# Kernel optimization log

Measured on AMD Instinct MI355X. Metric: run time of the kernel, lower is better.

The kernel has to match this reference:

```python
import jax, jax.numpy as jnp
import numpy as np

MIN_NORM = 1e-15
EPS = 1e-7
N_NODES = 100000
N_EDGES = 1600000
D_IN = 256
D_OUT = 128

# ---- Hyperboloid manifold ops (HGCN-style) ----

def proj_tan0(u, c):
    # zero out the time (first) coordinate
    return jnp.concatenate([jnp.zeros_like(u[..., :1]), u[..., 1:]], axis=-1)

def proj(x, c):
    # project onto hyperboloid: recompute time coord from space coords
    K = 1.0 / c
    y = x[..., 1:]
    t = jnp.sqrt(jnp.clip(K + jnp.sum(y * y, axis=-1, keepdims=True), EPS, None))
    return jnp.concatenate([t, y], axis=-1)

def expmap0(u, c):
    sqrtK = jnp.sqrt(1.0 / c)
    x = u[..., 1:]
    nrm = jnp.clip(jnp.linalg.norm(x, axis=-1, keepdims=True), MIN_NORM, None)
    theta = nrm / sqrtK
    t0 = sqrtK * jnp.cosh(theta)
    rest = sqrtK * jnp.sinh(theta) * x / nrm
    return proj(jnp.concatenate([t0, rest], axis=-1), c)

def logmap0(x, c):
    sqrtK = jnp.sqrt(1.0 / c)
    y = x[..., 1:]
    nrm = jnp.clip(jnp.linalg.norm(y, axis=-1, keepdims=True), MIN_NORM, None)
    theta = jnp.clip(x[..., :1] / sqrtK, 1.0 + EPS, None)
    rest = sqrtK * jnp.arccosh(theta) * y / nrm
    return jnp.concatenate([jnp.zeros_like(rest[..., :1]), rest], axis=-1)

def mobius_matvec1(m, x, c):
    # weight is (in, out): map via tangent space at origin
    return expmap0(logmap0(x, c) @ m, c)

def mobius_matvec0(n, x, c):
    # per-node scalar (N,1) scaling in tangent space
    return expmap0(n * logmap0(x, c), c)

def mobius_add(x, y, c):
    # tangent-space addition at origin (broadcasts over bias rows)
    return expmap0(logmap0(x, c) + logmap0(y, c), c)

mobius_add0 = mobius_add

def spmm(rows, cols, vals, x):
    # COO sparse adj @ dense x  ->  [N, d]
    return jax.ops.segment_sum(vals[:, None] * x[cols], rows, num_segments=N_NODES)

def gcn_layer(x, weight, bias, rows, cols, vals, c):
    out = mobius_matvec1(weight, x, c)
    hyp_bias = proj(expmap0(proj_tan0(bias[None, :], c), c), c)
    out = mobius_add(out, hyp_bias, c)
    out = logmap0(out, c)
    out = spmm(rows, cols, vals, out)
    return proj(expmap0(out, c), c)


def setup_inputs() -> dict:
    key = jax.random.key(0)
    ks = jax.random.split(key, 12)
    A1_tensor = jax.random.normal(ks[0], (N_NODES, D_IN), dtype=jnp.float32)
    adj_rows = jax.random.randint(ks[1], (N_EDGES,), 0, N_NODES)
    adj_cols = jax.random.randint(ks[2], (N_EDGES,), 0, N_NODES)
    adj_vals = jax.random.uniform(ks[3], (N_EDGES,), dtype=jnp.float32) / 16.0
    raw_c = jnp.full((1,), np.log(np.e - 1.0), dtype=jnp.float32)
    bnd_in = 1.0 / np.sqrt(D_IN)
    bnd_h = 1.0 / np.sqrt(D_OUT)
    Lin1 = jax.random.uniform(ks[4], (D_IN, D_OUT), jnp.float32, -bnd_in, bnd_in)
    Lin1_bias = jax.random.uniform(ks[5], (D_OUT,), jnp.float32, -bnd_in, bnd_in)
    n = jax.random.uniform(ks[6], (N_NODES, 1), jnp.float32, 0.0, 1.0)
    gc1_weight = jax.random.uniform(ks[7], (D_IN, D_OUT), jnp.float32, -bnd_in, bnd_in)
    gc1_bias = jax.random.uniform(ks[8], (D_OUT,), jnp.float32, -bnd_in, bnd_in)
    gc2_weight = jax.random.uniform(ks[9], (D_OUT, D_OUT), jnp.float32, -bnd_h, bnd_h)
    gc2_bias = jax.random.uniform(ks[10], (D_OUT,), jnp.float32, -bnd_h, bnd_h)
    return {"A1_tensor": A1_tensor, "adj_rows": adj_rows, "adj_cols": adj_cols,
            "adj_vals": adj_vals, "raw_c": raw_c, "Lin1": Lin1, "Lin1_bias": Lin1_bias,
            "n": n, "gc1_weight": gc1_weight, "gc1_bias": gc1_bias,
            "gc2_weight": gc2_weight, "gc2_bias": gc2_bias}


def reference(A1_tensor, adj_rows, adj_cols, adj_vals, raw_c, Lin1, Lin1_bias, n,
              gc1_weight, gc1_bias, gc2_weight, gc2_bias):
    c = jax.nn.softplus(raw_c) + 1e-5  # learned curvature, shape (1,)
    # dropout is identity at inference
    x_tan = proj_tan0(A1_tensor, c)
    a = proj(expmap0(x_tan, c), c)
    # skip branch: hyperbolic linear
    a1 = mobius_matvec1(Lin1, a, c)
    hyp_bias = proj(expmap0(proj_tan0(Lin1_bias[None, :], c), c), c)
    a1 = mobius_add(a1, hyp_bias, c)
    a2 = mobius_matvec0(n, a1, c)
    # GCN layer 1 + gated residual
    x_1 = gcn_layer(a, gc1_weight, gc1_bias, adj_rows, adj_cols, adj_vals, c)
    x_1 = mobius_matvec0(1.0 - n, x_1, c)
    x_1 = mobius_add0(x_1, a2, c)
    # GCN layer 2
    x_2 = gcn_layer(x_1, gc2_weight, gc2_bias, adj_rows, adj_cols, adj_vals, c)
    x_2 = logmap0(x_2, c)
    x_2 = jnp.concatenate([x_2, a1], axis=-1)  # [N, 2*D_OUT]
    x_2 = expmap0(x_2, c)
    return (x_2, c)
```

## Files before the change

kernel.cpp:

```cpp
#include <hip/hip_runtime.h>
#include <math.h>


#define NN 100000
#define MAXDEG 64
#define NB 391
#define CAP 5120
#define EPT 16
#define EPB 4096

typedef __attribute__((ext_vector_type(8))) short bf16x8;
typedef __attribute__((ext_vector_type(4))) float f32x4;

__device__ __forceinline__ float wsum(float v) {
#pragma unroll
  for (int off = 32; off > 0; off >>= 1) v += __shfl_xor(v, off, 64);
  return v;
}

__device__ __forceinline__ float sane(float v) {
  return fminf(fmaxf(v, -3.0e38f), 3.0e38f);
}

__device__ __forceinline__ float b2f(ushort h) {
  union { unsigned u; float f; } z; z.u = (unsigned)h << 16; return z.f;
}
__device__ __forceinline__ ushort f2b(float f) {
  union { float f; unsigned u; } z; z.f = f;
  unsigned u = z.u;
  unsigned r = (u + 0x7fffu + ((u >> 16) & 1u)) >> 16;
  return (ushort)r;
}

__global__ __launch_bounds__(256) void prep_kernel(const float* __restrict__ Lin1,
                                                   const float* __restrict__ g1w,
                                                   const float* __restrict__ g2w,
                                                   ushort* __restrict__ Bt1,
                                                   ushort* __restrict__ Btg1,
                                                   ushort* __restrict__ Btg2,
                                                   int* __restrict__ bucketCnt,
                                                   const float* __restrict__ raw_c,
                                                   float* __restrict__ SC) {
  int i = blockIdx.x * 256 + threadIdx.x;
  if (i < 32768) {
    int k = i >> 7, n = i & 127;
    Bt1[n * 256 + k] = f2b(Lin1[i]);
  } else if (i < 65536) {
    int j = i - 32768, k = j >> 7, n = j & 127;
    Btg1[n * 256 + k] = f2b(g1w[j]);
  } else if (i < 81920) {
    int j = i - 65536, k = j >> 7, n = j & 127;
    Btg2[n * 128 + k] = f2b(g2w[j]);
  } else if (i < 81920 + NB) {
    bucketCnt[i - 81920] = 0;
  } else if (i == 81920 + NB) {
    float rc = raw_c[0];
    float c = fmaxf(rc, 0.0f) + log1pf(expf(-fabsf(rc))) + 1e-5f;
    SC[0] = c;
    SC[1] = 1.0f / c;
    SC[2] = sqrtf(1.0f / c);
    SC[3] = sqrtf(c);
  }
}

__global__ __launch_bounds__(256) void convA_kernel(const float* __restrict__ A1,
                                                    ushort* __restrict__ A1h) {
  long i = (long)blockIdx.x * 256 + threadIdx.x;
  const long total = (long)NN * 256 / 8;
  if (i >= total) return;
  const float* p = A1 + i * 8;
  float4 v0 = *(const float4*)p;
  float4 v1 = *(const float4*)(p + 4);
  ushort t[8] = {f2b(v0.x), f2b(v0.y), f2b(v0.z), f2b(v0.w),
                 f2b(v1.x), f2b(v1.y), f2b(v1.z), f2b(v1.w)};
  if (((i * 8) & 255) == 0) t[0] = 0;
  *(uint4*)(A1h + i * 8) = *(uint4*)t;
}

__global__ __launch_bounds__(256) void mfma_gemm_kernel(const ushort* __restrict__ A, int lda,
                                                        const ushort* __restrict__ Bt,
                                                        ushort* __restrict__ C,
                                                        const float* __restrict__ bias,
                                                        int M, int K) {
  __shared__ ushort As[128][40];
  __shared__ ushort Bs[128][40];
  const int tid = threadIdx.x;
  const int w = tid >> 6, l = tid & 63;
  const int wr = w >> 1, wc = w & 1;
  const int lane16 = l & 15, quad = l >> 4;
  const int bm = blockIdx.x * 128;
  f32x4 acc[4][4];
#pragma unroll
  for (int mt = 0; mt < 4; ++mt)
#pragma unroll
    for (int nt = 0; nt < 4; ++nt) acc[mt][nt] = (f32x4){0.f, 0.f, 0.f, 0.f};

  for (int k0 = 0; k0 < K; k0 += 32) {
#pragma unroll
    for (int p = 0; p < 2; ++p) {
      int idx = p * 256 + tid;
      int row = idx >> 2;
      int kc = (idx & 3) * 8;
      int grow = bm + row;
      uint4 av = make_uint4(0, 0, 0, 0);
      if (grow < M) av = *(const uint4*)(A + (size_t)grow * lda + k0 + kc);
      *(uint4*)(&As[row][kc]) = av;
      uint4 bv = *(const uint4*)(Bt + (size_t)row * K + k0 + kc);
      *(uint4*)(&Bs[row][kc]) = bv;
    }
    __syncthreads();
    bf16x8 af[4], bfr[4];
#pragma unroll
    for (int mt = 0; mt < 4; ++mt)
      af[mt] = *(const bf16x8*)(&As[wr * 64 + mt * 16 + lane16][quad * 8]);
#pragma unroll
    for (int nt = 0; nt < 4; ++nt)
      bfr[nt] = *(const bf16x8*)(&Bs[wc * 64 + nt * 16 + lane16][quad * 8]);
#pragma unroll
    for (int mt = 0; mt < 4; ++mt)
#pragma unroll
      for (int nt = 0; nt < 4; ++nt)
        acc[mt][nt] = __builtin_amdgcn_mfma_f32_16x16x32_bf16(af[mt], bfr[nt], acc[mt][nt], 0, 0, 0);
    __syncthreads();
  }
#pragma unroll
  for (int mt = 0; mt < 4; ++mt) {
#pragma unroll
    for (int r = 0; r < 4; ++r) {
      int row = bm + wr * 64 + mt * 16 + quad * 4 + r;
      if (row < M) {
#pragma unroll
        for (int nt = 0; nt < 4; ++nt) {
          int col = wc * 64 + nt * 16 + lane16;
          float v = acc[mt][nt][r] + ((col == 0) ? 0.0f : bias[col]);
          C[(size_t)row * 128 + col] = f2b(v);
        }
      }
    }
  }
}

__global__ __launch_bounds__(256) void part1_kernel(const int* __restrict__ rows,
                                                    const int* __restrict__ cols,
                                                    const float* __restrict__ vals,
                                                    int* __restrict__ bucketCnt,
                                                    uint2* __restrict__ store, int E) {
  __shared__ int hist[NB];
  __shared__ int cursor[NB];
  const int tid = threadIdx.x;
  for (int t = tid; t < NB; t += 256) hist[t] = 0;
  __syncthreads();
  const long base = (long)blockIdx.x * EPB;
  int rw[EPT];
  unsigned pk[EPT];
#pragma unroll
  for (int k = 0; k < EPT; ++k) {
    long i = base + (long)k * 256 + tid;
    rw[k] = -1;
    if (i < E) {
      rw[k] = rows[i];
      pk[k] = ((unsigned)cols[i] << 15) | ((unsigned)f2b(vals[i]) & 0x7FFFu);
      atomicAdd(&hist[rw[k] >> 8], 1);
    }
  }
  __syncthreads();
  for (int t = tid; t < NB; t += 256) {
    int h = hist[t];
    cursor[t] = (h > 0) ? atomicAdd(&bucketCnt[t], h) : 0;
  }
  __syncthreads();
#pragma unroll
  for (int k = 0; k < EPT; ++k) {
    if (rw[k] >= 0) {
      int b = rw[k] >> 8;
      int pos = atomicAdd(&cursor[b], 1);
      if (pos < CAP) store[(size_t)b * CAP + pos] = make_uint2(pk[k], (unsigned)rw[k]);
    }
  }
}

__global__ __launch_bounds__(256) void part2_kernel(const int* __restrict__ bucketCnt,
                                                    const uint2* __restrict__ store,
                                                    int* __restrict__ deg,
                                                    unsigned* __restrict__ eCV) {
  __shared__ int d2[256];
  const int b = blockIdx.x, tid = threadIdx.x;
  d2[tid] = 0;
  __syncthreads();
  int n = bucketCnt[b];
  n = (n > CAP) ? CAP : n;
  const uint2* bs = store + (size_t)b * CAP;
  for (int i = tid; i < n; i += 256) {
    uint2 rec = bs[i];
    int rl = rec.y & 255;
    int k = atomicAdd(&d2[rl], 1);
    if (k < MAXDEG) eCV[((size_t)rec.y << 6) + k] = rec.x;
  }
  __syncthreads();
  int gr = b * 256 + tid;
  if (gr < NN) deg[gr] = d2[tid];
}

__device__ __forceinline__ void row_gather(int row, int l,
                                           const int* __restrict__ deg,
                                           const unsigned* __restrict__ eCV,
                                           const ushort* __restrict__ Gh,
                                           float& a0, float& a1) {
  unsigned mine = eCV[(size_t)row * MAXDEG + l];
  int dg = __builtin_amdgcn_readfirstlane(deg[row]);
  dg = (dg > MAXDEG) ? MAXDEG : dg;
  a0 = 0.0f; a1 = 0.0f;
  const int lo = l << 1;
  for (int j = 0; j < dg; j += 16) {
    unsigned pj[16];
    ushort2 u[16];
#pragma unroll
    for (int q = 0; q < 16; ++q) {
      int kk = j + q;
      kk = (kk < dg) ? kk : (dg - 1);
      pj[q] = (unsigned)__builtin_amdgcn_readlane((int)mine, kk);
      u[q] = *(const ushort2*)(Gh + ((size_t)(pj[q] >> 15) << 7) + lo);
    }
#pragma unroll
    for (int q = 0; q < 16; ++q) {
      union { unsigned u32; float f; } vv;
      vv.u32 = (j + q < dg) ? ((pj[q] & 0x7FFFu) << 16) : 0u;
      a0 = fmaf(vv.f, b2f(u[q].x), a0);
      a1 = fmaf(vv.f, b2f(u[q].y), a1);
    }
  }
}

__global__ __launch_bounds__(256) void spmm1_kernel(const int* __restrict__ deg,
                                                    const unsigned* __restrict__ eCV,
                                                    const ushort* __restrict__ G1h,
                                                    const ushort* __restrict__ Pb,
                                                    const float* __restrict__ nvec,
                                                    const float* __restrict__ SC,
                                                    ushort* __restrict__ TBh,
                                                    ushort* __restrict__ A1Ph) {
  int row = __builtin_amdgcn_readfirstlane(blockIdx.x * 4 + (threadIdx.x >> 6));
  int l = threadIdx.x & 63;
  if (row >= NN) return;
  float sK = SC[2], rsK = SC[3];
  float nval = nvec[row];
  float a0, a1;
  row_gather(row, l, deg, eCV, G1h, a0, a1);
  ushort2 pu = *(const ushort2*)(Pb + (size_t)row * 128 + 2 * l);
  float p0 = b2f(pu.x), p1 = b2f(pu.y);
  float t10 = (l == 0) ? 0.0f : fmaf(1.0f - nval, a0, nval * p0);
  float t11 = fmaf(1.0f - nval, a1, nval * p1);
  ushort2 tb; tb.x = f2b(t10); tb.y = f2b(t11);
  *(ushort2*)(TBh + (size_t)row * 128 + 2 * l) = tb;
  float px = (l == 0) ? 0.0f : p0;
  float py = p1;
  float ss = wsum(px * px + py * py);
  float rinv = fminf(__builtin_amdgcn_rsqf(ss), 1e15f);
  float nrm = ss * rinv;
  float th = nrm * rsK;
  float e = __expf(th);
  float ei = __builtin_amdgcn_rcpf(e);
  float sh = 0.5f * (e - ei), ch = 0.5f * (e + ei);
  float sc = sK * sh * rinv;
  float t = sK * ch;
  ushort2 st;
  st.x = f2b((l == 0) ? t : sc * px);
  st.y = f2b(sc * py);
  *(ushort2*)(A1Ph + (size_t)row * 128 + 2 * l) = st;
}

__global__ __launch_bounds__(256) void spmm2_kernel(const int* __restrict__ deg,
                                                    const unsigned* __restrict__ eCV,
                                                    const ushort* __restrict__ G2h,
                                                    const ushort* __restrict__ A1Ph,
                                                    const float* __restrict__ SC,
                                                    float* __restrict__ out) {
  int row = __builtin_amdgcn_readfirstlane(blockIdx.x * 4 + (threadIdx.x >> 6));
  int l = threadIdx.x & 63;
  if (row >= NN) return;
  float cval = SC[0], K = SC[1], sK = SC[2], rsK = SC[3];
  float a0, a1;
  row_gather(row, l, deg, eCV, G2h, a0, a1);
  float u0 = (l == 0) ? 0.0f : a0;
  float u1 = a1;
  ushort2 ap = *(const ushort2*)(A1Ph + (size_t)row * 128 + 2 * l);
  float u2 = b2f(ap.x), u3 = b2f(ap.y);
  float ss = wsum(u0 * u0 + u1 * u1 + u2 * u2 + u3 * u3);
  float rinv = fminf(__builtin_amdgcn_rsqf(ss), 1e15f);
  float nrm = ss * rinv;
  float th = nrm * rsK;
  float e = __expf(th);
  float ei = __builtin_amdgcn_rcpf(e);
  float sc = sK * (0.5f * (e - ei)) * rinv;
  float o0 = sc * u0, o1 = sc * u1, o2 = sc * u2, o3 = sc * u3;
  if (l == 0) o0 = 0.0f;
  float t2 = sqrtf(fmaxf(K + sc * sc * ss, 1e-7f));
  float* op = out + (size_t)row * 256;
  float2 w0, w1;
  w0.x = sane((l == 0) ? t2 : o0);
  w0.y = sane(o1);
  w1.x = sane(o2);
  w1.y = sane(o3);
  *(float2*)(op + 2 * l) = w0;
  *(float2*)(op + 128 + 2 * l) = w1;
  if (row == 0 && l == 0) out[(size_t)NN * 256] = cval;
}

extern "C" void kernel_launch(void* const* d_in, const int* in_sizes, int n_in,
                              void* d_out, int out_size, void* d_ws, size_t ws_size,
                              hipStream_t stream) {
  const float* A1  = (const float*)d_in[0];
  const int* rows  = (const int*)d_in[1];
  const int* cols  = (const int*)d_in[2];
  const float* vals = (const float*)d_in[3];
  const float* rawc = (const float*)d_in[4];
  const float* Lin1 = (const float*)d_in[5];
  const float* Lb   = (const float*)d_in[6];
  const float* nv   = (const float*)d_in[7];
  const float* g1w  = (const float*)d_in[8];
  const float* g1b  = (const float*)d_in[9];
  const float* g2w  = (const float*)d_in[10];
  const float* g2b  = (const float*)d_in[11];
  float* out = (float*)d_out;
  float* ws = (float*)d_ws;
  const int E = in_sizes[1];

  float*  SC   = ws;
  ushort* A1h  = (ushort*)(ws + 256);
  ushort* Pb   = A1h + (size_t)256 * NN;
  ushort* G1h  = Pb + (size_t)128 * NN;
  ushort* TBh  = G1h + (size_t)128 * NN;
  ushort* A1Ph = TBh + (size_t)128 * NN;
  ushort* Bt1  = A1Ph + (size_t)128 * NN;
  ushort* Btg1 = Bt1 + 128 * 256;
  ushort* Btg2 = Btg1 + 128 * 256;
  int* deg      = (int*)(Btg2 + 128 * 256);
  unsigned* eCV = (unsigned*)(deg + 100096);
  uint2* store   = (uint2*)A1Ph;
  int* bucketCnt = (int*)(store + (size_t)NB * CAP);

  const int rowBlocks = (NN + 3) / 4;
  const int gemmGrid = (NN + 127) / 128;
  const int p1Blocks = (E + EPB - 1) / EPB;
  const int prepBlocks = (81920 + NB + 1 + 255) / 256;

  prep_kernel<<<prepBlocks, 256, 0, stream>>>(Lin1, g1w, g2w, Bt1, Btg1, Btg2,
                                              bucketCnt, rawc, SC);
  part1_kernel<<<p1Blocks, 256, 0, stream>>>(rows, cols, vals, bucketCnt, store, E);
  part2_kernel<<<NB, 256, 0, stream>>>(bucketCnt, store, deg, eCV);

  convA_kernel<<<(NN * 256 / 8 + 255) / 256, 256, 0, stream>>>(A1, A1h);
  mfma_gemm_kernel<<<gemmGrid, 256, 0, stream>>>(A1h, 256, Bt1, Pb, Lb, NN, 256);
  mfma_gemm_kernel<<<gemmGrid, 256, 0, stream>>>(A1h, 256, Btg1, G1h, g1b, NN, 256);
  spmm1_kernel<<<rowBlocks, 256, 0, stream>>>(deg, eCV, G1h, Pb, nv, SC, TBh, A1Ph);
  mfma_gemm_kernel<<<gemmGrid, 256, 0, stream>>>(TBh, 128, Btg2, G1h, g2b, NN, 128);
  spmm2_kernel<<<rowBlocks, 256, 0, stream>>>(deg, eCV, G1h, A1Ph, SC, out);
}
```

Before: 462.5 us.

## Pad rows, use direct global-to-LDS loads with swizzle, pad edge lists, tune partitioning

Node arrays are padded to a multiple of 128 rows (zero-filled), so the GEMM can drop its bounds checks and load tiles with global_load_lds into an XOR-swizzled LDS layout. The MFMA operands are swapped so each lane stores a contiguous ushort4 row chunk with a vectorized bias load. Per-row edge lists are padded with zero entries to a multiple of 16, which removes the clamp and select logic in the gather loop. The partition kernels change their per-thread edge count and part2 block size. The extra padded memory, the zeroing work and the swizzle indexing add some risk.

```diff
diff --git a/kernel.cpp b/kernel.cpp
--- a/kernel.cpp
+++ b/kernel.cpp
@@ -3,11 +3,12 @@
 
 
 #define NN 100000
+#define NP 100096
 #define MAXDEG 64
 #define NB 391
 #define CAP 5120
-#define EPT 16
-#define EPB 4096
+#define EPT 8
+#define EPB 2048
 
 typedef __attribute__((ext_vector_type(8))) short bf16x8;
 typedef __attribute__((ext_vector_type(4))) float f32x4;
@@ -30,6 +31,11 @@
   unsigned u = z.u;
   unsigned r = (u + 0x7fffu + ((u >> 16) & 1u)) >> 16;
   return (ushort)r;
+}
+
+__device__ __forceinline__ void gload16(const void* g, void* l) {
+  __builtin_amdgcn_global_load_lds((const __attribute__((address_space(1))) void*)g,
+                                   (__attribute__((address_space(3))) void*)l, 16, 0, 0);
 }
 
 __global__ __launch_bounds__(256) void prep_kernel(const float* __restrict__ Lin1,
@@ -40,7 +46,8 @@
                                                    ushort* __restrict__ Btg2,
                                                    int* __restrict__ bucketCnt,
                                                    const float* __restrict__ raw_c,
-                                                   float* __restrict__ SC) {
+                                                   float* __restrict__ SC,
+                                                   ushort* __restrict__ TBh) {
   int i = blockIdx.x * 256 + threadIdx.x;
   if (i < 32768) {
     int k = i >> 7, n = i & 127;
@@ -60,14 +67,22 @@
     SC[1] = 1.0f / c;
     SC[2] = sqrtf(1.0f / c);
     SC[3] = sqrtf(c);
+  } else if (i >= 90000 && i < 90000 + 6144) {
+    ((unsigned*)(TBh + (size_t)NN * 128))[i - 90000] = 0u;
   }
 }
 
 __global__ __launch_bounds__(256) void convA_kernel(const float* __restrict__ A1,
                                                     ushort* __restrict__ A1h) {
   long i = (long)blockIdx.x * 256 + threadIdx.x;
-  const long total = (long)NN * 256 / 8;
+  const long total = (long)NP * 32;
   if (i >= total) return;
+  long row = i >> 5;
+  if (row >= NN) {
+    uint4 z = make_uint4(0, 0, 0, 0);
+    *(uint4*)(A1h + i * 8) = z;
+    return;
+  }
   const float* p = A1 + i * 8;
   float4 v0 = *(const float4*)p;
   float4 v1 = *(const float4*)(p + 4);
@@ -81,14 +96,15 @@
                                                         const ushort* __restrict__ Bt,
                                                         ushort* __restrict__ C,
                                                         const float* __restrict__ bias,
-                                                        int M, int K) {
-  __shared__ ushort As[128][40];
-  __shared__ ushort Bs[128][40];
+                                                        int K) {
+  __shared__ ushort As[128 * 32];
+  __shared__ ushort Bs[128 * 32];
   const int tid = threadIdx.x;
   const int w = tid >> 6, l = tid & 63;
   const int wr = w >> 1, wc = w & 1;
   const int lane16 = l & 15, quad = l >> 4;
   const int bm = blockIdx.x * 128;
+  const int swz = (lane16 >> 1) & 3;
   f32x4 acc[4][4];
 #pragma unroll
   for (int mt = 0; mt < 4; ++mt)
@@ -98,44 +114,44 @@
   for (int k0 = 0; k0 < K; k0 += 32) {
 #pragma unroll
     for (int p = 0; p < 2; ++p) {
-      int idx = p * 256 + tid;
-      int row = idx >> 2;
-      int kc = (idx & 3) * 8;
-      int grow = bm + row;
-      uint4 av = make_uint4(0, 0, 0, 0);
-      if (grow < M) av = *(const uint4*)(A + (size_t)grow * lda + k0 + kc);
-      *(uint4*)(&As[row][kc]) = av;
-      uint4 bv = *(const uint4*)(Bt + (size_t)row * K + k0 + kc);
-      *(uint4*)(&Bs[row][kc]) = bv;
+      int sseg = p * 256 + tid;
+      int row = sseg >> 2;
+      int kq = (sseg & 3) ^ ((row >> 1) & 3);
+      int wbase = (p * 256 + (tid & ~63)) * 16;
+      gload16(A + (size_t)(bm + row) * lda + k0 + kq * 8, (char*)As + wbase);
+      gload16(Bt + (size_t)row * K + k0 + kq * 8, (char*)Bs + wbase);
     }
     __syncthreads();
     bf16x8 af[4], bfr[4];
 #pragma unroll
     for (int mt = 0; mt < 4; ++mt)
-      af[mt] = *(const bf16x8*)(&As[wr * 64 + mt * 16 + lane16][quad * 8]);
+      af[mt] = *(const bf16x8*)((const char*)As +
+                (size_t)(wr * 64 + mt * 16 + lane16) * 64 + ((quad ^ swz) * 16));
 #pragma unroll
     for (int nt = 0; nt < 4; ++nt)
-      bfr[nt] = *(const bf16x8*)(&Bs[wc * 64 + nt * 16 + lane16][quad * 8]);
+      bfr[nt] = *(const bf16x8*)((const char*)Bs +
+                 (size_t)(wc * 64 + nt * 16 + lane16) * 64 + ((quad ^ swz) * 16));
 #pragma unroll
     for (int mt = 0; mt < 4; ++mt)
 #pragma unroll
       for (int nt = 0; nt < 4; ++nt)
-        acc[mt][nt] = __builtin_amdgcn_mfma_f32_16x16x32_bf16(af[mt], bfr[nt], acc[mt][nt], 0, 0, 0);
+        acc[mt][nt] = __builtin_amdgcn_mfma_f32_16x16x32_bf16(bfr[nt], af[mt], acc[mt][nt], 0, 0, 0);
     __syncthreads();
   }
 #pragma unroll
-  for (int mt = 0; mt < 4; ++mt) {
-#pragma unroll
-    for (int r = 0; r < 4; ++r) {
-      int row = bm + wr * 64 + mt * 16 + quad * 4 + r;
-      if (row < M) {
-#pragma unroll
-        for (int nt = 0; nt < 4; ++nt) {
-          int col = wc * 64 + nt * 16 + lane16;
-          float v = acc[mt][nt][r] + ((col == 0) ? 0.0f : bias[col]);
-          C[(size_t)row * 128 + col] = f2b(v);
-        }
-      }
+  for (int nt = 0; nt < 4; ++nt) {
+    int colb = wc * 64 + nt * 16 + quad * 4;
+    float4 b4 = *(const float4*)(bias + colb);
+    if (colb == 0) b4.x = 0.0f;
+#pragma unroll
+    for (int mt = 0; mt < 4; ++mt) {
+      int row = bm + wr * 64 + mt * 16 + lane16;
+      ushort4 st;
+      st.x = f2b(acc[mt][nt][0] + b4.x);
+      st.y = f2b(acc[mt][nt][1] + b4.y);
+      st.z = f2b(acc[mt][nt][2] + b4.z);
+      st.w = f2b(acc[mt][nt][3] + b4.w);
+      *(ushort4*)(C + (size_t)row * 128 + colb) = st;
     }
   }
 }
@@ -151,18 +167,17 @@
   for (int t = tid; t < NB; t += 256) hist[t] = 0;
   __syncthreads();
   const long base = (long)blockIdx.x * EPB;
-  int rw[EPT];
-  unsigned pk[EPT];
+  int rw[EPT], ck[EPT];
+  float vf[EPT];
 #pragma unroll
   for (int k = 0; k < EPT; ++k) {
     long i = base + (long)k * 256 + tid;
     rw[k] = -1;
-    if (i < E) {
-      rw[k] = rows[i];
-      pk[k] = ((unsigned)cols[i] << 15) | ((unsigned)f2b(vals[i]) & 0x7FFFu);
-      atomicAdd(&hist[rw[k] >> 8], 1);
-    }
-  }
+    if (i < E) { rw[k] = rows[i]; ck[k] = cols[i]; vf[k] = vals[i]; }
+  }
+#pragma unroll
+  for (int k = 0; k < EPT; ++k)
+    if (rw[k] >= 0) atomicAdd(&hist[rw[k] >> 8], 1);
   __syncthreads();
   for (int t = tid; t < NB; t += 256) {
     int h = hist[t];
@@ -174,31 +189,40 @@
     if (rw[k] >= 0) {
       int b = rw[k] >> 8;
       int pos = atomicAdd(&cursor[b], 1);
-      if (pos < CAP) store[(size_t)b * CAP + pos] = make_uint2(pk[k], (unsigned)rw[k]);
-    }
-  }
-}
-
-__global__ __launch_bounds__(256) void part2_kernel(const int* __restrict__ bucketCnt,
-                                                    const uint2* __restrict__ store,
-                                                    int* __restrict__ deg,
-                                                    unsigned* __restrict__ eCV) {
+      unsigned pk = ((unsigned)ck[k] << 15) | ((unsigned)f2b(vf[k]) & 0x7FFFu);
+      if (pos < CAP) store[(size_t)b * CAP + pos] = make_uint2(pk, (unsigned)rw[k]);
+    }
+  }
+}
+
+__global__ __launch_bounds__(1024) void part2_kernel(const int* __restrict__ bucketCnt,
+                                                     const uint2* __restrict__ store,
+                                                     int* __restrict__ deg,
+                                                     unsigned* __restrict__ eCV) {
   __shared__ int d2[256];
   const int b = blockIdx.x, tid = threadIdx.x;
-  d2[tid] = 0;
+  if (tid < 256) d2[tid] = 0;
   __syncthreads();
   int n = bucketCnt[b];
   n = (n > CAP) ? CAP : n;
   const uint2* bs = store + (size_t)b * CAP;
-  for (int i = tid; i < n; i += 256) {
+  for (int i = tid; i < n; i += 1024) {
     uint2 rec = bs[i];
     int rl = rec.y & 255;
     int k = atomicAdd(&d2[rl], 1);
     if (k < MAXDEG) eCV[((size_t)rec.y << 6) + k] = rec.x;
   }
   __syncthreads();
-  int gr = b * 256 + tid;
-  if (gr < NN) deg[gr] = d2[tid];
+  if (tid < 256) {
+    int gr = b * 256 + tid;
+    if (gr < NN) {
+      int dgv = d2[tid];
+      dgv = (dgv > MAXDEG) ? MAXDEG : dgv;
+      int pe = (dgv + 15) & ~15;
+      for (int k = dgv; k < pe; ++k) eCV[((size_t)gr << 6) + k] = 0u;
+      deg[gr] = pe;
+    }
+  }
 }
 
 __device__ __forceinline__ void row_gather(int row, int l,
@@ -208,7 +232,6 @@
                                            float& a0, float& a1) {
   unsigned mine = eCV[(size_t)row * MAXDEG + l];
   int dg = __builtin_amdgcn_readfirstlane(deg[row]);
-  dg = (dg > MAXDEG) ? MAXDEG : dg;
   a0 = 0.0f; a1 = 0.0f;
   const int lo = l << 1;
   for (int j = 0; j < dg; j += 16) {
@@ -216,15 +239,12 @@
     ushort2 u[16];
 #pragma unroll
     for (int q = 0; q < 16; ++q) {
-      int kk = j + q;
-      kk = (kk < dg) ? kk : (dg - 1);
-      pj[q] = (unsigned)__builtin_amdgcn_readlane((int)mine, kk);
+      pj[q] = (unsigned)__builtin_amdgcn_readlane((int)mine, j + q);
       u[q] = *(const ushort2*)(Gh + ((size_t)(pj[q] >> 15) << 7) + lo);
     }
 #pragma unroll
     for (int q = 0; q < 16; ++q) {
-      union { unsigned u32; float f; } vv;
-      vv.u32 = (j + q < dg) ? ((pj[q] & 0x7FFFu) << 16) : 0u;
+      union { unsigned u32; float f; } vv; vv.u32 = (pj[q] & 0x7FFFu) << 16;
       a0 = fmaf(vv.f, b2f(u[q].x), a0);
       a1 = fmaf(vv.f, b2f(u[q].y), a1);
     }
@@ -327,32 +347,32 @@
 
   float*  SC   = ws;
   ushort* A1h  = (ushort*)(ws + 256);
-  ushort* Pb   = A1h + (size_t)256 * NN;
-  ushort* G1h  = Pb + (size_t)128 * NN;
-  ushort* TBh  = G1h + (size_t)128 * NN;
-  ushort* A1Ph = TBh + (size_t)128 * NN;
-  ushort* Bt1  = A1Ph + (size_t)128 * NN;
+  ushort* Pb   = A1h + (size_t)256 * NP;
+  ushort* G1h  = Pb + (size_t)128 * NP;
+  ushort* TBh  = G1h + (size_t)128 * NP;
+  ushort* A1Ph = TBh + (size_t)128 * NP;
+  ushort* Bt1  = A1Ph + (size_t)128 * NP;
   ushort* Btg1 = Bt1 + 128 * 256;
   ushort* Btg2 = Btg1 + 128 * 256;
   int* deg      = (int*)(Btg2 + 128 * 256);
-  unsigned* eCV = (unsigned*)(deg + 100096);
+  unsigned* eCV = (unsigned*)(deg + NP);
   uint2* store   = (uint2*)A1Ph;
   int* bucketCnt = (int*)(store + (size_t)NB * CAP);
 
-  const int rowBlocks = (NN + 3) / 4;
-  const int gemmGrid = (NN + 127) / 128;
+  const int rowBlocks = NN / 4;
+  const int gemmGrid = NP / 128;
   const int p1Blocks = (E + EPB - 1) / EPB;
-  const int prepBlocks = (81920 + NB + 1 + 255) / 256;
+  const int prepBlocks = (90000 + 6144 + 255) / 256;
 
   prep_kernel<<<prepBlocks, 256, 0, stream>>>(Lin1, g1w, g2w, Bt1, Btg1, Btg2,
-                                              bucketCnt, rawc, SC);
+                                              bucketCnt, rawc, SC, TBh);
   part1_kernel<<<p1Blocks, 256, 0, stream>>>(rows, cols, vals, bucketCnt, store, E);
-  part2_kernel<<<NB, 256, 0, stream>>>(bucketCnt, store, deg, eCV);
-
-  convA_kernel<<<(NN * 256 / 8 + 255) / 256, 256, 0, stream>>>(A1, A1h);
-  mfma_gemm_kernel<<<gemmGrid, 256, 0, stream>>>(A1h, 256, Bt1, Pb, Lb, NN, 256);
-  mfma_gemm_kernel<<<gemmGrid, 256, 0, stream>>>(A1h, 256, Btg1, G1h, g1b, NN, 256);
+  part2_kernel<<<NB, 1024, 0, stream>>>(bucketCnt, store, deg, eCV);
+
+  convA_kernel<<<(NP * 32 + 255) / 256, 256, 0, stream>>>(A1, A1h);
+  mfma_gemm_kernel<<<gemmGrid, 256, 0, stream>>>(A1h, 256, Bt1, Pb, Lb, 256);
+  mfma_gemm_kernel<<<gemmGrid, 256, 0, stream>>>(A1h, 256, Btg1, G1h, g1b, 256);
   spmm1_kernel<<<rowBlocks, 256, 0, stream>>>(deg, eCV, G1h, Pb, nv, SC, TBh, A1Ph);
-  mfma_gemm_kernel<<<gemmGrid, 256, 0, stream>>>(TBh, 128, Btg2, G1h, g2b, NN, 128);
+  mfma_gemm_kernel<<<gemmGrid, 256, 0, stream>>>(TBh, 128, Btg2, G1h, g2b, 128);
   spmm2_kernel<<<rowBlocks, 256, 0, stream>>>(deg, eCV, G1h, A1Ph, SC, out);
 }
```

Measured after the change: 457.0 us. No clear change (-1.2%).
